# Optimization experiments

Hardware: AMD Instinct MI355X
Metric: run time of the kernel (lower is better)

## Reference

```python
import jax, jax.numpy as jnp
import numpy as np

N, D, E, H, K = 4096, 512, 32, 128, 4  # tokens, d_model, n_experts, expert hidden, top-k


def setup_inputs() -> dict:
    key = jax.random.key(0)
    k0, k1, k2, k3 = jax.random.split(key, 4)
    x = jax.random.normal(k0, (N, D), dtype=jnp.float32)
    # router weights, init std = d**-0.5 (matches get_initializer std)
    expert_sel = jax.random.normal(k1, (E, D), dtype=jnp.float32) * (D ** -0.5)
    # per-expert MLP weights (Linear stores [out, in]; we keep [E, in, out] layout)
    w1 = jax.random.normal(k2, (E, D, H), dtype=jnp.float32) * (D ** -0.5)
    w2 = jax.random.normal(k3, (E, H, D), dtype=jnp.float32) * (H ** -0.5)
    return {"x": x, "expert_sel": expert_sel, "w1": w1, "w2": w2}


def reference(x, expert_sel, w1, w2):
    # routing: sigmoid selection, top-k experts per token
    scores = jax.nn.sigmoid(x @ expert_sel.T)          # [N, E]
    gate_vals, gate_idx = jax.lax.top_k(scores, K)     # [N, K]
    # dense gate matrix with only top-k nonzero (sparse dispatch/combine weights)
    gate = (jax.nn.one_hot(gate_idx, E, dtype=x.dtype) * gate_vals[..., None]).sum(-2)  # [N, E]
    # per-expert MLP; gating at hidden is exact since experts have no bias:
    # gate * (relu(x W1) W2) == (gate * relu(x W1)) W2
    h = jax.nn.relu(jnp.einsum('nd,edh->neh', x, w1)) * gate[..., None]  # [N, E, H]
    y = jnp.einsum('neh,ehv->nv', h, w2)               # [N, D]
    return y
```

## Files before the change

kernel.cpp:

```cpp
#include <hip/hip_runtime.h>
#include <hip/hip_bf16.h>

#define NTOK 4096
#define DM   512
#define NE   32
#define HD   128
#define TK   4

typedef unsigned short u16;
typedef unsigned int   u32;
typedef u16   u16x4 __attribute__((ext_vector_type(4)));
typedef u16   u16x8 __attribute__((ext_vector_type(8)));
typedef short short8 __attribute__((ext_vector_type(8)));
typedef float f32x4 __attribute__((ext_vector_type(4)));

__device__ __forceinline__ u16 f2bf(float f) {
    union { float f; u32 u; } v; v.f = f;
    return (u16)((v.u + 0x7FFFu + ((v.u >> 16) & 1u)) >> 16);
}
__device__ __forceinline__ float bf2f(u16 h) {
    union { u32 u; float f; } v; v.u = ((u32)h) << 16; return v.f;
}

__global__ __launch_bounds__(256) void swizzle_kernel(const float* __restrict__ w1,
                                                      const float* __restrict__ w2,
                                                      u16* __restrict__ wf1,
                                                      u16* __restrict__ wf2) {
    int tid = threadIdx.x;
    int wv = tid >> 6, lane = tid & 63;
    int m = lane & 15, q = lane >> 4;
    int f0 = (blockIdx.x * 4 + wv) * 2;

    const float* in[2]; u16* outp[2]; int Nd[2];
#pragma unroll
    for (int u = 0; u < 2; ++u) {
        int w = f0 + u;
        if (w < 4096) {
            int e = w >> 7, rem = w & 127, ks = rem >> 3, nt = rem & 7;
            in[u] = w1 + (size_t)e * DM * HD + (size_t)(32 * ks + q * 8) * HD + 16 * nt + m;
            Nd[u] = HD;
            outp[u] = wf1 + (size_t)w * 512 + lane * 8;
        } else {
            int wl = w - 4096, e = wl >> 7, rem = wl & 127, ks = rem >> 5, nt = rem & 31;
            in[u] = w2 + (size_t)e * HD * DM + (size_t)(32 * ks + q * 8) * DM + 16 * nt + m;
            Nd[u] = DM;
            outp[u] = wf2 + (size_t)wl * 512 + lane * 8;
        }
    }
    float v[2][8];
#pragma unroll
    for (int u = 0; u < 2; ++u)
#pragma unroll
        for (int j = 0; j < 8; ++j) v[u][j] = in[u][(size_t)j * Nd[u]];
#pragma unroll
    for (int u = 0; u < 2; ++u) {
        u16x8 h;
#pragma unroll
        for (int j = 0; j < 8; ++j) h[j] = f2bf(v[u][j]);
        *(u16x8*)outp[u] = h;
    }
}

__global__ __launch_bounds__(256) void router_kernel(const float* __restrict__ x,
                                                     const float* __restrict__ sel,
                                                     u32* __restrict__ route_e,
                                                     float* __restrict__ route_g,
                                                     u16* __restrict__ xbf) {
    __shared__ float  sl[32][516];
    __shared__ float  xs[4][520];
    __shared__ double sc[4][33];
    int tid = threadIdx.x;
    int tb = blockIdx.x * 4;

#pragma unroll
    for (int rep = 0; rep < 16; ++rep) {
        int idx = (rep * 256 + tid) * 4;
        int row = idx >> 9, col = idx & 511;
        *(f32x4*)&sl[row][col] = *(const f32x4*)(sel + idx);
    }
#pragma unroll
    for (int rep = 0; rep < 2; ++rep) {
        int idx = (rep * 256 + tid) * 4;
        int row = idx >> 9, col = idx & 511;
        f32x4 v = *(const f32x4*)(x + (size_t)(tb + row) * DM + col);
        *(f32x4*)&xs[row][col] = v;
        u16x4 h;
#pragma unroll
        for (int j = 0; j < 4; ++j) h[j] = f2bf(v[j]);
        *(u16x4*)(xbf + (size_t)(tb + row) * DM + col) = h;
    }
    __syncthreads();

    int tok = tid & 3, seg = (tid >> 2) & 1, e = tid >> 3;
    const float* sp = &sl[e][seg * 256];
    const float* xp = &xs[tok][seg * 256];
    double pa = 0.0, pb = 0.0, pc = 0.0, pd = 0.0;
#pragma unroll 4
    for (int j = 0; j < 256; j += 16) {
        f32x4 x0 = *(const f32x4*)(xp + j);
        f32x4 x1 = *(const f32x4*)(xp + j + 4);
        f32x4 x2 = *(const f32x4*)(xp + j + 8);
        f32x4 x3 = *(const f32x4*)(xp + j + 12);
        f32x4 s0 = *(const f32x4*)(sp + j);
        f32x4 s1 = *(const f32x4*)(sp + j + 4);
        f32x4 s2 = *(const f32x4*)(sp + j + 8);
        f32x4 s3 = *(const f32x4*)(sp + j + 12);
#pragma unroll
        for (int k = 0; k < 4; ++k) {
            pa = fma((double)x0[k], (double)s0[k], pa);
            pb = fma((double)x1[k], (double)s1[k], pb);
            pc = fma((double)x2[k], (double)s2[k], pc);
            pd = fma((double)x3[k], (double)s3[k], pd);
        }
    }
    double p = (pa + pb) + (pc + pd);
    p += __shfl_xor(p, 4);
    if (seg == 0) sc[tok][e] = p;
    __syncthreads();

    if (tid < 4) {
        int t = tb + tid;
        unsigned mask = 0;
        u32 eids = 0;
        f32x4 gs;
        for (int k = 0; k < TK; ++k) {
            double best = -1e300; int be = 0;
            for (int ee = 0; ee < NE; ++ee) {
                double v = sc[tid][ee];
                if (!((mask >> ee) & 1u) && v > best) { best = v; be = ee; }
            }
            mask |= 1u << be;
            eids |= (u32)be << (8 * k);
            gs[k] = 1.0f / (1.0f + __expf(-(float)best));
        }
        route_e[t] = eids;
        *(f32x4*)&route_g[4 * t] = gs;
    }
}

__global__ __launch_bounds__(256) void build_kernel(const u32* __restrict__ route_e,
                                                    const float* __restrict__ route_g,
                                                    int* __restrict__ counts,
                                                    int* __restrict__ tok_list,
                                                    float* __restrict__ gate_list) {
    int e = blockIdx.x;
    __shared__ int cnt;
    if (threadIdx.x == 0) cnt = 0;
    __syncthreads();
#pragma unroll
    for (int rep = 0; rep < NTOK / 256; ++rep) {
        int t = rep * 256 + threadIdx.x;
        u32 eid = route_e[t];
        int k = -1;
        if ((eid & 255u) == (u32)e) k = 0;
        else if (((eid >> 8) & 255u) == (u32)e) k = 1;
        else if (((eid >> 16) & 255u) == (u32)e) k = 2;
        else if (((eid >> 24) & 255u) == (u32)e) k = 3;
        if (k >= 0) {
            int pos = atomicAdd(&cnt, 1);
            tok_list[e * NTOK + pos]  = (k << 16) | t;
            gate_list[e * NTOK + pos] = route_g[4 * t + k];
        }
    }
    __syncthreads();
    if (threadIdx.x == 0) counts[e] = cnt;
}

__global__ __launch_bounds__(256, 2) void moe_mlp_kernel(const u16* __restrict__ xbf,
                                                         const u16* __restrict__ wf1,
                                                         const u16* __restrict__ wf2,
                                                         const int* __restrict__ counts,
                                                         const int* __restrict__ tok_list,
                                                         const float* __restrict__ gate_list,
                                                         u16* __restrict__ part,
                                                         float* __restrict__ out,
                                                         int use_part) {
    __shared__ int   s_cnt[NE];
    __shared__ int   s_ent[64];
    __shared__ float s_gate[64];
    __shared__ __align__(16) u16 Hm[64][136];

    int tid = threadIdx.x;
    if (tid < NE) s_cnt[tid] = counts[tid];
    __syncthreads();

    int b = blockIdx.x;
    int e = -1, t = 0, rows = 0, pre = 0;
#pragma unroll 8
    for (int ee = 0; ee < NE; ++ee) {
        int cc = s_cnt[ee];
        int nt = (cc + 63) >> 6;
        if (e < 0 && b < pre + nt) { e = ee; t = b - pre; rows = cc - t * 64; if (rows > 64) rows = 64; }
        pre += nt;
    }
    if (e < 0) return;

    if (tid < 64) {
        int base = e * NTOK + t * 64;
        bool val = tid < rows;
        s_ent[tid]  = tok_list[base + (val ? tid : 0)];
        s_gate[tid] = val ? gate_list[base + tid] : 0.0f;
    }
    __syncthreads();

    int wv = tid >> 6, lane = tid & 63, m = lane & 15, q = lane >> 4;
    int r = wv >> 1, c = wv & 1;
    const u16* w1f = wf1 + (size_t)e * (128 * 512);
    const u16* w2f = wf2 + (size_t)e * (128 * 512);

    const u16* a0 = xbf + (size_t)(s_ent[32 * r + m] & 0xFFFF) * DM + q * 8;
    const u16* a1 = xbf + (size_t)(s_ent[32 * r + 16 + m] & 0xFFFF) * DM + q * 8;

    short8 ab[2][2][2];
    short8 bb[2][2][4];
#pragma unroll
    for (int kk = 0; kk < 2; ++kk) {
        ab[0][kk][0] = *(const short8*)(a0 + 32 * kk);
        ab[0][kk][1] = *(const short8*)(a1 + 32 * kk);
        const u16* bp = w1f + (size_t)kk * 4096 + (size_t)(4 * c) * 512 + lane * 8;
#pragma unroll
        for (int n = 0; n < 4; ++n) bb[0][kk][n] = *(const short8*)(bp + n * 512);
    }
    f32x4 acc[2][4];
#pragma unroll
    for (int i = 0; i < 2; ++i)
#pragma unroll
        for (int n = 0; n < 4; ++n) acc[i][n] = (f32x4){0.f, 0.f, 0.f, 0.f};

#pragma unroll
    for (int kp = 0; kp < 8; ++kp) {
        int cur = kp & 1, nxt = cur ^ 1;
        if (kp < 7) {
            int ks0 = 2 * (kp + 1);
#pragma unroll
            for (int kk = 0; kk < 2; ++kk) {
                ab[nxt][kk][0] = *(const short8*)(a0 + 32 * (ks0 + kk));
                ab[nxt][kk][1] = *(const short8*)(a1 + 32 * (ks0 + kk));
                const u16* bp = w1f + (size_t)(ks0 + kk) * 4096 + (size_t)(4 * c) * 512 + lane * 8;
#pragma unroll
                for (int n = 0; n < 4; ++n) bb[nxt][kk][n] = *(const short8*)(bp + n * 512);
            }
        }
#pragma unroll
        for (int kk = 0; kk < 2; ++kk)
#pragma unroll
            for (int i = 0; i < 2; ++i)
#pragma unroll
                for (int n = 0; n < 4; ++n)
                    acc[i][n] = __builtin_amdgcn_mfma_f32_16x16x32_bf16(ab[cur][kk][i],
                                                                        bb[cur][kk][n],
                                                                        acc[i][n], 0, 0, 0);
    }

#pragma unroll
    for (int i = 0; i < 2; ++i) {
        int rb = 32 * r + 16 * i + q * 4;
#pragma unroll
        for (int n = 0; n < 4; ++n)
#pragma unroll
            for (int rr = 0; rr < 4; ++rr)
                Hm[rb + rr][64 * c + 16 * n + m] =
                    f2bf(fmaxf(acc[i][n][rr], 0.f) * s_gate[rb + rr]);
    }

    short8 cb[4][8];
#pragma unroll
    for (int ks = 0; ks < 4; ++ks) {
        const u16* bp = w2f + (size_t)(ks * 32 + wv * 8) * 512 + lane * 8;
#pragma unroll
        for (int n = 0; n < 8; ++n) cb[ks][n] = *(const short8*)(bp + n * 512);
    }
    __syncthreads();

#pragma unroll
    for (int half = 0; half < 2; ++half) {
        f32x4 acc2[2][8];
#pragma unroll
        for (int i = 0; i < 2; ++i)
#pragma unroll
            for (int n = 0; n < 8; ++n) acc2[i][n] = (f32x4){0.f, 0.f, 0.f, 0.f};
#pragma unroll
        for (int ks = 0; ks < 4; ++ks) {
            short8 h0 = *(const short8*)&Hm[32 * half + m][32 * ks + q * 8];
            short8 h1 = *(const short8*)&Hm[32 * half + 16 + m][32 * ks + q * 8];
#pragma unroll
            for (int n = 0; n < 8; ++n) {
                acc2[0][n] = __builtin_amdgcn_mfma_f32_16x16x32_bf16(h0, cb[ks][n], acc2[0][n], 0, 0, 0);
                acc2[1][n] = __builtin_amdgcn_mfma_f32_16x16x32_bf16(h1, cb[ks][n], acc2[1][n], 0, 0, 0);
            }
        }
#pragma unroll
        for (int i = 0; i < 2; ++i) {
            int rb = 32 * half + 16 * i + q * 4;
#pragma unroll
            for (int rr = 0; rr < 4; ++rr) {
                int rl = rb + rr;
                if (rl < rows) {
                    int en = s_ent[rl];
                    int tk = en & 0xFFFF, sl = en >> 16;
                    if (use_part) {
                        u16* pp = part + ((size_t)sl * NTOK + tk) * DM + 128 * wv + m;
#pragma unroll
                        for (int n = 0; n < 8; ++n) pp[16 * n] = f2bf(acc2[i][n][rr]);
                    } else {
                        float* op = out + (size_t)tk * DM + 128 * wv + m;
#pragma unroll
                        for (int n = 0; n < 8; ++n) atomicAdd(&op[16 * n], acc2[i][n][rr]);
                    }
                }
            }
        }
    }
}

__global__ __launch_bounds__(256) void combine_kernel(const u16* __restrict__ part,
                                                      float* __restrict__ out) {
    size_t off = ((size_t)blockIdx.x * 256 + threadIdx.x) * 8;
    float s[8] = {0, 0, 0, 0, 0, 0, 0, 0};
#pragma unroll
    for (int k = 0; k < TK; ++k) {
        u16x8 p = *(const u16x8*)(part + (size_t)k * NTOK * DM + off);
#pragma unroll
        for (int j = 0; j < 8; ++j) s[j] += bf2f(p[j]);
    }
    *(f32x4*)(out + off)     = (f32x4){s[0], s[1], s[2], s[3]};
    *(f32x4*)(out + off + 4) = (f32x4){s[4], s[5], s[6], s[7]};
}

extern "C" void kernel_launch(void* const* d_in, const int* in_sizes, int n_in,
                              void* d_out, int out_size, void* d_ws, size_t ws_size,
                              hipStream_t stream) {
    const float* x   = (const float*)d_in[0];
    const float* sel = (const float*)d_in[1];
    const float* w1  = (const float*)d_in[2];
    const float* w2  = (const float*)d_in[3];
    float* out = (float*)d_out;

    char* ws = (char*)d_ws;
    int*   counts    = (int*)(ws);
    u32*   route_e   = (u32*)(ws + 256);
    float* route_g   = (float*)(ws + 256 + (size_t)NTOK * 4);
    char*  ws2       = ws + 256 + (size_t)NTOK * 20;
    int*   tok_list  = (int*)(ws2);
    float* gate_list = (float*)(ws2 + (size_t)NE * NTOK * 4);
    u16*   xbf  = (u16*)(ws2 + (size_t)NE * NTOK * 8);
    u16*   wf1  = xbf + (size_t)NTOK * DM;
    u16*   wf2  = wf1 + (size_t)NE * HD * DM;
    u16*   part = wf2 + (size_t)NE * HD * DM;

    size_t need = 256 + (size_t)NTOK * 20 + (size_t)NE * NTOK * 8
                + (size_t)NTOK * DM * 2 + 2 * (size_t)NE * HD * DM * 2
                + (size_t)TK * NTOK * DM * 2;
    int use_part = (ws_size >= need) ? 1 : 0;

    if (!use_part)
        hipMemsetAsync(d_out, 0, (size_t)NTOK * DM * sizeof(float), stream);

    swizzle_kernel<<<1024, 256, 0, stream>>>(w1, w2, wf1, wf2);
    router_kernel<<<NTOK / 4, 256, 0, stream>>>(x, sel, route_e, route_g, xbf);
    build_kernel<<<NE, 256, 0, stream>>>(route_e, route_g, counts, tok_list, gate_list);
    moe_mlp_kernel<<<288, 256, 0, stream>>>(xbf, wf1, wf2, counts, tok_list, gate_list,
                                            part, out, use_part);
    if (use_part)
        combine_kernel<<<NTOK * DM / 8 / 256, 256, 0, stream>>>(part, out);
}
```

Measured before the change: 136.8 us.

## Stage MoE output tile in LDS for vectorized row stores; XCD-aware expert mapping

```diff
diff --git a/kernel.cpp b/kernel.cpp
--- a/kernel.cpp
+++ b/kernel.cpp
@@ -179,18 +179,21 @@
     __shared__ int   s_ent[64];
     __shared__ float s_gate[64];
     __shared__ __align__(16) u16 Hm[64][136];
+    __shared__ __align__(16) u16 Ct[32][520];
 
     int tid = threadIdx.x;
     if (tid < NE) s_cnt[tid] = counts[tid];
     __syncthreads();
 
     int b = blockIdx.x;
+    int xcd = b & 7, idx = b >> 3;
     int e = -1, t = 0, rows = 0, pre = 0;
-#pragma unroll 8
-    for (int ee = 0; ee < NE; ++ee) {
+#pragma unroll
+    for (int j = 0; j < 4; ++j) {
+        int ee = xcd + 8 * j;
         int cc = s_cnt[ee];
         int nt = (cc + 63) >> 6;
-        if (e < 0 && b < pre + nt) { e = ee; t = b - pre; rows = cc - t * 64; if (rows > 64) rows = 64; }
+        if (e < 0 && idx < pre + nt) { e = ee; t = idx - pre; rows = cc - t * 64; if (rows > 64) rows = 64; }
         pre += nt;
     }
     if (e < 0) return;
@@ -291,25 +294,32 @@
         }
 #pragma unroll
         for (int i = 0; i < 2; ++i) {
-            int rb = 32 * half + 16 * i + q * 4;
-#pragma unroll
-            for (int rr = 0; rr < 4; ++rr) {
-                int rl = rb + rr;
-                if (rl < rows) {
-                    int en = s_ent[rl];
-                    int tk = en & 0xFFFF, sl = en >> 16;
-                    if (use_part) {
-                        u16* pp = part + ((size_t)sl * NTOK + tk) * DM + 128 * wv + m;
-#pragma unroll
-                        for (int n = 0; n < 8; ++n) pp[16 * n] = f2bf(acc2[i][n][rr]);
-                    } else {
-                        float* op = out + (size_t)tk * DM + 128 * wv + m;
-#pragma unroll
-                        for (int n = 0; n < 8; ++n) atomicAdd(&op[16 * n], acc2[i][n][rr]);
-                    }
+            int rb = 16 * i + q * 4;
+#pragma unroll
+            for (int n = 0; n < 8; ++n)
+#pragma unroll
+                for (int rr = 0; rr < 4; ++rr)
+                    Ct[rb + rr][128 * wv + 16 * n + m] = f2bf(acc2[i][n][rr]);
+        }
+        __syncthreads();
+#pragma unroll
+        for (int rep = 0; rep < 8; ++rep) {
+            int rl = rep * 4 + wv;
+            int rt = 32 * half + rl;
+            u16x8 v = *(const u16x8*)&Ct[rl][lane * 8];
+            if (rt < rows) {
+                int en = s_ent[rt];
+                int tk = en & 0xFFFF, sl2 = en >> 16;
+                if (use_part) {
+                    *(u16x8*)(part + ((size_t)sl2 * NTOK + tk) * DM + lane * 8) = v;
+                } else {
+                    float* op = out + (size_t)tk * DM + lane * 8;
+#pragma unroll
+                    for (int j = 0; j < 8; ++j) atomicAdd(&op[j], bf2f(v[j]));
                 }
             }
         }
+        __syncthreads();
     }
 }
 
@@ -359,8 +369,8 @@
     swizzle_kernel<<<1024, 256, 0, stream>>>(w1, w2, wf1, wf2);
     router_kernel<<<NTOK / 4, 256, 0, stream>>>(x, sel, route_e, route_g, xbf);
     build_kernel<<<NE, 256, 0, stream>>>(route_e, route_g, counts, tok_list, gate_list);
-    moe_mlp_kernel<<<288, 256, 0, stream>>>(xbf, wf1, wf2, counts, tok_list, gate_list,
-                                            part, out, use_part);
+    moe_mlp_kernel<<<2080, 256, 0, stream>>>(xbf, wf1, wf2, counts, tok_list, gate_list,
+                                             part, out, use_part);
     if (use_part)
         combine_kernel<<<NTOK * DM / 8 / 256, 256, 0, stream>>>(part, out);
 }
```

After: 133.1 us. -2.7%, faster.
